# Performance work log

Hardware: AMD Instinct MI355X
Metric: run time of the kernel (lower is better)

The kernel has to match this reference:

```python
import jax, jax.numpy as jnp
import numpy as np

N, E, G = 50000, 800000, 64
IN_DIM, HID, HEADS = 128, 64, 4
EPS = 1e-5
NEG_SLOPE = 0.2


def _gatv2(x, src, dst, Wl, bl, Wr, br, att, bias, heads, ch):
    n = x.shape[0]
    xl = (x @ Wl + bl).reshape(n, heads, ch)
    xr = (x @ Wr + br).reshape(n, heads, ch)
    # edge-wise gather + GATv2 attention logits
    e = jax.nn.leaky_relu(xl[src] + xr[dst], NEG_SLOPE)          # [E,H,C]
    logits = jnp.einsum('ehc,hc->eh', e, att)                    # [E,H]
    # segment softmax over incoming edges of each destination node
    m = jax.ops.segment_max(logits, dst, num_segments=n)
    a = jnp.exp(logits - m[dst])
    denom = jax.ops.segment_sum(a, dst, num_segments=n)
    alpha = a / denom[dst]                                       # [E,H]
    out = jax.ops.segment_sum(alpha[:, :, None] * xl[src], dst, num_segments=n)
    return out.reshape(n, heads * ch) + bias


def _batchnorm(x, gamma, beta):
    mu = jnp.mean(x, axis=0)
    var = jnp.var(x, axis=0)
    return gamma * (x - mu) * jax.lax.rsqrt(var + EPS) + beta


def setup_inputs() -> dict:
    key = jax.random.key(0)
    ks = jax.random.split(key, 24)
    d1 = HID * HEADS  # 256
    def g(k, shape, scale):
        return jax.random.normal(k, shape, dtype=jnp.float32) * scale
    return {
        'x': g(ks[0], (N, IN_DIM), 1.0),
        'edge_index': jax.random.randint(ks[1], (2, E), 0, N, dtype=jnp.int32),
        'batch': jnp.sort(jax.random.randint(ks[2], (N,), 0, G, dtype=jnp.int32)),
        # conv1
        'W1l': g(ks[3], (IN_DIM, d1), 0.08), 'b1l': jnp.zeros((d1,), jnp.float32),
        'W1r': g(ks[4], (IN_DIM, d1), 0.08), 'b1r': jnp.zeros((d1,), jnp.float32),
        'att1': g(ks[5], (HEADS, HID), 0.1), 'bias1': jnp.zeros((d1,), jnp.float32),
        'gamma1': jnp.ones((d1,), jnp.float32), 'beta1': jnp.zeros((d1,), jnp.float32),
        # conv2 (heads=1)
        'W2l': g(ks[6], (d1, HID), 0.06), 'b2l': jnp.zeros((HID,), jnp.float32),
        'W2r': g(ks[7], (d1, HID), 0.06), 'b2r': jnp.zeros((HID,), jnp.float32),
        'att2': g(ks[8], (1, HID), 0.1), 'bias2': jnp.zeros((HID,), jnp.float32),
        'gamma2': jnp.ones((HID,), jnp.float32), 'beta2': jnp.zeros((HID,), jnp.float32),
        # MLP head
        'lw1': g(ks[9], (HID, HID), 0.12), 'lb1': jnp.zeros((HID,), jnp.float32),
        'lw2': g(ks[10], (HID, 1), 0.12), 'lb2': jnp.zeros((1,), jnp.float32),
    }


def reference(x, edge_index, batch, W1l, b1l, W1r, b1r, att1, bias1, gamma1, beta1,
              W2l, b2l, W2r, b2r, att2, bias2, gamma2, beta2, lw1, lb1, lw2, lb2):
    n = x.shape[0]
    loops = jnp.arange(n, dtype=edge_index.dtype)
    src = jnp.concatenate([edge_index[0], loops])
    dst = jnp.concatenate([edge_index[1], loops])

    h = _gatv2(x, src, dst, W1l, b1l, W1r, b1r, att1, bias1, HEADS, HID)
    h = jax.nn.elu(_batchnorm(h, gamma1, beta1))
    # dropout: identity in eval mode
    h = _gatv2(h, src, dst, W2l, b2l, W2r, b2r, att2, bias2, 1, HID)
    h = jax.nn.elu(_batchnorm(h, gamma2, beta2))

    # global mean pool over graphs
    sums = jax.ops.segment_sum(h, batch, num_segments=G)
    cnts = jax.ops.segment_sum(jnp.ones((n, 1), h.dtype), batch, num_segments=G)
    pooled = sums / jnp.maximum(cnts, 1.0)

    out = jax.nn.elu(pooled @ lw1 + lb1)
    return out @ lw2 + lb2
```

## Files before the change

kernel.cpp:

```cpp
#include <hip/hip_runtime.h>
#include <hip/hip_bf16.h>

#define NN 50000
#define NE 800000
#define ET (NE + NN)
#define NG 64
#define IND 128
#define HD 64
#define NH 4
#define D1 256
#define BN_EPS 1e-5f
#define SLOPE 0.2f
#define PW_NODES 25
#define LOG2E 1.4426950408889634f

typedef unsigned short u16;
typedef __attribute__((ext_vector_type(8))) short bf16x8;
typedef __attribute__((ext_vector_type(4))) float f32x4;

__device__ __forceinline__ float b2f(u16 u){
  union { unsigned int i; float f; } c; c.i = ((unsigned int)u) << 16; return c.f;
}
__device__ __forceinline__ u16 f2b(float f){
  unsigned int u = __float_as_uint(f);
  u = (u + 0x7FFF + ((u >> 16) & 1)) >> 16;
  return (u16)u;
}

__global__ void k_cvt(const float* __restrict__ x, u16* __restrict__ xb, int n4){
  int i = blockIdx.x*256 + threadIdx.x;
  if (i >= n4) return;
  float4 v = reinterpret_cast<const float4*>(x)[i];
  ushort4 o; o.x = f2b(v.x); o.y = f2b(v.y); o.z = f2b(v.z); o.w = f2b(v.w);
  reinterpret_cast<ushort4*>(xb)[i] = o;
}

__global__ void k_wprep(const float* __restrict__ Wa, const float* __restrict__ Wb,
                        u16* __restrict__ Wt, int KT, int NOUT){
  int id = blockIdx.x*256 + threadIdx.x;
  int total = 2*NOUT*(KT/4);
  if (id >= total) return;
  int c  = id % (2*NOUT);
  int k4 = (id / (2*NOUT))*4;
  const float* W = (c < NOUT) ? Wa : Wb;
  int cl = (c < NOUT) ? c : c - NOUT;
  ushort4 o;
  o.x = f2b(W[(size_t)(k4+0)*NOUT + cl]);
  o.y = f2b(W[(size_t)(k4+1)*NOUT + cl]);
  o.z = f2b(W[(size_t)(k4+2)*NOUT + cl]);
  o.w = f2b(W[(size_t)(k4+3)*NOUT + cl]);
  *reinterpret_cast<ushort4*>(&Wt[(size_t)c*KT + k4]) = o;
}

__global__ void k_count(const int* __restrict__ ei, int* __restrict__ cnt){
  int e = blockIdx.x*256 + threadIdx.x;
  if (e >= ET) return;
  int d = (e < NE) ? ei[NE + e] : (e - NE);
  atomicAdd(&cnt[d], 1);
}

__global__ __launch_bounds__(1024) void k_scan1(const int* __restrict__ cnt,
                                                int* __restrict__ ro, int* __restrict__ part){
  __shared__ int s[1024];
  int i = blockIdx.x*1024 + threadIdx.x;
  int v = (i < NN) ? cnt[i] : 0;
  s[threadIdx.x] = v;
  __syncthreads();
  for (int off = 1; off < 1024; off <<= 1){
    int t = (threadIdx.x >= off) ? s[threadIdx.x - off] : 0;
    __syncthreads();
    s[threadIdx.x] += t;
    __syncthreads();
  }
  if (i < NN) ro[i] = s[threadIdx.x] - v;
  if (threadIdx.x == 1023) part[blockIdx.x] = s[1023];
}

__global__ __launch_bounds__(64) void k_scan2(int* __restrict__ part, int nb){
  __shared__ int s[64];
  int v = (threadIdx.x < nb) ? part[threadIdx.x] : 0;
  s[threadIdx.x] = v;
  __syncthreads();
  for (int off = 1; off < 64; off <<= 1){
    int t = (threadIdx.x >= off) ? s[threadIdx.x - off] : 0;
    __syncthreads();
    s[threadIdx.x] += t;
    __syncthreads();
  }
  if (threadIdx.x < nb) part[threadIdx.x] = s[threadIdx.x] - v;
}

__global__ __launch_bounds__(1024) void k_scan3(const int* __restrict__ part, int* __restrict__ ro){
  int i = blockIdx.x*1024 + threadIdx.x;
  if (i < NN) ro[i] += part[blockIdx.x];
  if (i == 0) ro[NN] = ET;
}

__global__ void k_scatter(const int* __restrict__ ei, const int* __restrict__ ro,
                          int* __restrict__ cur, int* __restrict__ ssrc){
  int e = blockIdx.x*256 + threadIdx.x;
  if (e >= ET) return;
  int s, d;
  if (e < NE){ s = ei[e]; d = ei[NE + e]; } else { s = e - NE; d = s; }
  int pos = ro[d] + atomicAdd(&cur[d], 1);
  ssrc[pos] = s;
}

template<int KT, int NOUT>
__global__ __launch_bounds__(256) void k_gemm(const u16* __restrict__ Ab,
      const u16* __restrict__ Wt, const float* __restrict__ ba, const float* __restrict__ bb,
      u16* __restrict__ Ca, u16* __restrict__ Cb){
  __shared__ u16 As[64][32];
  __shared__ u16 Bs[128][32];
  int t = threadIdx.x;
  int lane = t & 63;
  int w = t >> 6;
  int wm = w >> 1, wn = w & 1;
  int n0 = blockIdx.x*64;
  int cb0 = blockIdx.y*128;

  f32x4 acc[2][4];
  #pragma unroll
  for (int i = 0; i < 2; i++)
    #pragma unroll
    for (int j = 0; j < 4; j++) acc[i][j] = (f32x4){0.f,0.f,0.f,0.f};

  int sr = t >> 3;
  int k4 = (t & 7)*4;
  int fm = lane & 15;
  int fk = (lane >> 4)*8;

  for (int kb = 0; kb < KT/32; kb++){
    int kbase = kb*32;
    #pragma unroll
    for (int p = 0; p < 2; p++){
      int r = sr + p*32;
      int gn = n0 + r;
      ushort4 v = make_ushort4(0,0,0,0);
      if (gn < NN) v = *reinterpret_cast<const ushort4*>(&Ab[(size_t)gn*KT + kbase + k4]);
      *reinterpret_cast<ushort4*>(&As[r][k4]) = v;
    }
    #pragma unroll
    for (int q = 0; q < 4; q++){
      int cn = sr + q*32;
      ushort4 v = *reinterpret_cast<const ushort4*>(&Wt[(size_t)(cb0+cn)*KT + kbase + k4]);
      *reinterpret_cast<ushort4*>(&Bs[cn][k4]) = v;
    }
    __syncthreads();
    bf16x8 af0 = *reinterpret_cast<const bf16x8*>(&As[wm*32 + fm][fk]);
    bf16x8 af1 = *reinterpret_cast<const bf16x8*>(&As[wm*32 + 16 + fm][fk]);
    #pragma unroll
    for (int nt = 0; nt < 4; nt++){
      bf16x8 bfr = *reinterpret_cast<const bf16x8*>(&Bs[wn*64 + nt*16 + fm][fk]);
      acc[0][nt] = __builtin_amdgcn_mfma_f32_16x16x32_bf16(af0, bfr, acc[0][nt], 0, 0, 0);
      acc[1][nt] = __builtin_amdgcn_mfma_f32_16x16x32_bf16(af1, bfr, acc[1][nt], 0, 0, 0);
    }
    __syncthreads();
  }

  int frow = (lane >> 4)*4;
  #pragma unroll
  for (int nt = 0; nt < 4; nt++){
    int cn = cb0 + wn*64 + nt*16 + fm;
    bool first = (cn < NOUT);
    int cl = first ? cn : cn - NOUT;
    float bv = first ? ba[cl] : bb[cl];
    u16* Cp = first ? Ca : Cb;
    #pragma unroll
    for (int mt = 0; mt < 2; mt++){
      #pragma unroll
      for (int r = 0; r < 4; r++){
        int grow = n0 + wm*32 + mt*16 + frow + r;
        if (grow < NN) Cp[(size_t)grow*NOUT + cl] = f2b(acc[mt][nt][r] + bv);
      }
    }
  }
}

__global__ __launch_bounds__(256) void k_gat1(const int* __restrict__ ro, const int* __restrict__ ssrc,
      const u16* __restrict__ xl, const u16* __restrict__ xr,
      const float* __restrict__ att, const float* __restrict__ bias,
      u16* __restrict__ out){
  int widx = threadIdx.x >> 6, lane = threadIdx.x & 63;
  int n = blockIdx.x*4 + widx;
  if (n >= NN) return;
  int base = (lane >> 4)*HD + (lane & 15)*4;
  ushort4 ur = *reinterpret_cast<const ushort4*>(&xr[(size_t)n*D1 + base]);
  float xr0 = b2f(ur.x), xr1 = b2f(ur.y), xr2 = b2f(ur.z), xr3 = b2f(ur.w);
  float4 at4 = *reinterpret_cast<const float4*>(&att[base]);
  float a1x = 0.6f*LOG2E*at4.x, a2x = 0.4f*LOG2E*at4.x;
  float a1y = 0.6f*LOG2E*at4.y, a2y = 0.4f*LOG2E*at4.y;
  float a1z = 0.6f*LOG2E*at4.z, a2z = 0.4f*LOG2E*at4.z;
  float a1w = 0.6f*LOG2E*at4.w, a2w = 0.4f*LOG2E*at4.w;
  float m = -1e30f, den = 0.f;
  float ax=0.f, ay=0.f, az=0.f, aw=0.f;
  int b = ro[n], e = ro[n+1];
  int i = b;
  for (; i + 3 < e; i += 4){
    int s0 = ssrc[i], s1 = ssrc[i+1], s2 = ssrc[i+2], s3 = ssrc[i+3];
    ushort4 u0 = *reinterpret_cast<const ushort4*>(&xl[(size_t)s0*D1 + base]);
    ushort4 u1 = *reinterpret_cast<const ushort4*>(&xl[(size_t)s1*D1 + base]);
    ushort4 u2 = *reinterpret_cast<const ushort4*>(&xl[(size_t)s2*D1 + base]);
    ushort4 u3 = *reinterpret_cast<const ushort4*>(&xl[(size_t)s3*D1 + base]);
    float v0x=b2f(u0.x), v0y=b2f(u0.y), v0z=b2f(u0.z), v0w=b2f(u0.w);
    float v1x=b2f(u1.x), v1y=b2f(u1.y), v1z=b2f(u1.z), v1w=b2f(u1.w);
    float v2x=b2f(u2.x), v2y=b2f(u2.y), v2z=b2f(u2.z), v2w=b2f(u2.w);
    float v3x=b2f(u3.x), v3y=b2f(u3.y), v3z=b2f(u3.z), v3w=b2f(u3.w);
    float t0, t1, t2, t3;
    float L0, L1, L2, L3;
    t0 = v0x+xr0; t1 = v0y+xr1; t2 = v0z+xr2; t3 = v0w+xr3;
    L0 = fmaf(a1x,t0, a2x*fabsf(t0));
    L0 = fmaf(a1y,t1, fmaf(a2y,fabsf(t1), L0));
    L0 = fmaf(a1z,t2, fmaf(a2z,fabsf(t2), L0));
    L0 = fmaf(a1w,t3, fmaf(a2w,fabsf(t3), L0));
    t0 = v1x+xr0; t1 = v1y+xr1; t2 = v1z+xr2; t3 = v1w+xr3;
    L1 = fmaf(a1x,t0, a2x*fabsf(t0));
    L1 = fmaf(a1y,t1, fmaf(a2y,fabsf(t1), L1));
    L1 = fmaf(a1z,t2, fmaf(a2z,fabsf(t2), L1));
    L1 = fmaf(a1w,t3, fmaf(a2w,fabsf(t3), L1));
    t0 = v2x+xr0; t1 = v2y+xr1; t2 = v2z+xr2; t3 = v2w+xr3;
    L2 = fmaf(a1x,t0, a2x*fabsf(t0));
    L2 = fmaf(a1y,t1, fmaf(a2y,fabsf(t1), L2));
    L2 = fmaf(a1z,t2, fmaf(a2z,fabsf(t2), L2));
    L2 = fmaf(a1w,t3, fmaf(a2w,fabsf(t3), L2));
    t0 = v3x+xr0; t1 = v3y+xr1; t2 = v3z+xr2; t3 = v3w+xr3;
    L3 = fmaf(a1x,t0, a2x*fabsf(t0));
    L3 = fmaf(a1y,t1, fmaf(a2y,fabsf(t1), L3));
    L3 = fmaf(a1z,t2, fmaf(a2z,fabsf(t2), L3));
    L3 = fmaf(a1w,t3, fmaf(a2w,fabsf(t3), L3));
    #pragma unroll
    for (int off = 1; off <= 8; off <<= 1){
      L0 += __shfl_xor(L0, off); L1 += __shfl_xor(L1, off);
      L2 += __shfl_xor(L2, off); L3 += __shfl_xor(L3, off);
    }
    float Lm = fmaxf(fmaxf(L0, L1), fmaxf(L2, L3));
    if (__any(Lm > m + 8.f)){
      float mn = fmaxf(m, Lm);
      float corr = exp2f(m - mn);
      den *= corr; ax *= corr; ay *= corr; az *= corr; aw *= corr;
      m = mn;
    }
    float p0 = exp2f(L0 - m), p1 = exp2f(L1 - m);
    float p2 = exp2f(L2 - m), p3 = exp2f(L3 - m);
    den += (p0 + p1) + (p2 + p3);
    ax = fmaf(p0,v0x, fmaf(p1,v1x, fmaf(p2,v2x, fmaf(p3,v3x, ax))));
    ay = fmaf(p0,v0y, fmaf(p1,v1y, fmaf(p2,v2y, fmaf(p3,v3y, ay))));
    az = fmaf(p0,v0z, fmaf(p1,v1z, fmaf(p2,v2z, fmaf(p3,v3z, az))));
    aw = fmaf(p0,v0w, fmaf(p1,v1w, fmaf(p2,v2w, fmaf(p3,v3w, aw))));
  }
  for (; i < e; i++){
    int s = ssrc[i];
    ushort4 u = *reinterpret_cast<const ushort4*>(&xl[(size_t)s*D1 + base]);
    float vx = b2f(u.x), vy = b2f(u.y), vz = b2f(u.z), vw = b2f(u.w);
    float t0 = vx + xr0, t1 = vy + xr1, t2 = vz + xr2, t3 = vw + xr3;
    float L;
    L = fmaf(a1x, t0, a2x*fabsf(t0));
    L = fmaf(a1y, t1, fmaf(a2y, fabsf(t1), L));
    L = fmaf(a1z, t2, fmaf(a2z, fabsf(t2), L));
    L = fmaf(a1w, t3, fmaf(a2w, fabsf(t3), L));
    L += __shfl_xor(L, 1); L += __shfl_xor(L, 2);
    L += __shfl_xor(L, 4); L += __shfl_xor(L, 8);
    if (__any(L > m + 8.f)){
      float mn = fmaxf(m, L);
      float corr = exp2f(m - mn);
      den *= corr; ax *= corr; ay *= corr; az *= corr; aw *= corr;
      m = mn;
    }
    float p = exp2f(L - m);
    den += p;
    ax = fmaf(p, vx, ax);
    ay = fmaf(p, vy, ay);
    az = fmaf(p, vz, az);
    aw = fmaf(p, vw, aw);
  }
  float inv = 1.f/den;
  float4 b4 = *reinterpret_cast<const float4*>(&bias[base]);
  ushort4 o;
  o.x = f2b(ax*inv + b4.x); o.y = f2b(ay*inv + b4.y);
  o.z = f2b(az*inv + b4.z); o.w = f2b(aw*inv + b4.w);
  *reinterpret_cast<ushort4*>(&out[(size_t)n*D1 + base]) = o;
}

__global__ __launch_bounds__(256) void k_bnstats16(const u16* __restrict__ h, float* __restrict__ stats,
                                                   int ncols, int rpb){
  int nrl = 256/ncols;
  int c = threadIdx.x % ncols;
  int rl = threadIdx.x / ncols;
  int r0 = blockIdx.x*rpb + rl;
  int r1 = min(NN, (blockIdx.x+1)*rpb);
  float s = 0.f, s2 = 0.f;
  for (int r = r0; r < r1; r += nrl){
    float v = b2f(h[(size_t)r*ncols + c]);
    s += v; s2 += v*v;
  }
  atomicAdd(&stats[c], s);
  atomicAdd(&stats[ncols + c], s2);
}

__global__ __launch_bounds__(256) void k_bnstats(const float* __restrict__ h, float* __restrict__ stats,
                                                 int ncols, int rpb){
  int nrl = 256/ncols;
  int c = threadIdx.x % ncols;
  int rl = threadIdx.x / ncols;
  int r0 = blockIdx.x*rpb + rl;
  int r1 = min(NN, (blockIdx.x+1)*rpb);
  float s = 0.f, s2 = 0.f;
  for (int r = r0; r < r1; r += nrl){
    float v = h[(size_t)r*ncols + c];
    s += v; s2 += v*v;
  }
  atomicAdd(&stats[c], s);
  atomicAdd(&stats[ncols + c], s2);
}

__global__ void k_bn1b(u16* __restrict__ h, const float* __restrict__ stats,
                       const float* __restrict__ gamma, const float* __restrict__ beta){
  const float invn = 1.f/NN;
  size_t total = (size_t)NN*D1/4;
  for (size_t i = (size_t)blockIdx.x*blockDim.x + threadIdx.x; i < total;
       i += (size_t)gridDim.x*blockDim.x){
    int c4 = (int)((i & (D1/4 - 1))*4);
    ushort4 u = reinterpret_cast<ushort4*>(h)[i];
    ushort4 o;
    #pragma unroll
    for (int j = 0; j < 4; j++){
      int c = c4 + j;
      float mu = stats[c]*invn;
      float var = stats[D1 + c]*invn - mu*mu;
      float g = gamma[c]*rsqrtf(var + BN_EPS);
      u16 uj = (j==0)?u.x:(j==1)?u.y:(j==2)?u.z:u.w;
      float v = (b2f(uj) - mu)*g + beta[c];
      v = (v > 0.f) ? v : (__expf(v) - 1.f);
      u16 ov = f2b(v);
      if (j==0) o.x = ov; else if (j==1) o.y = ov; else if (j==2) o.z = ov; else o.w = ov;
    }
    reinterpret_cast<ushort4*>(h)[i] = o;
  }
}

__global__ __launch_bounds__(256) void k_gat2(const int* __restrict__ ro, const int* __restrict__ ssrc,
      const u16* __restrict__ xl, const u16* __restrict__ xr,
      const float* __restrict__ att, const float* __restrict__ bias,
      float* __restrict__ out){
  int widx = threadIdx.x >> 6, lane = threadIdx.x & 63;
  int n = blockIdx.x*4 + widx;
  if (n >= NN) return;
  int g = lane >> 4, c4 = (lane & 15)*4;
  ushort4 ur = *reinterpret_cast<const ushort4*>(&xr[(size_t)n*HD + c4]);
  float xr0 = b2f(ur.x), xr1 = b2f(ur.y), xr2 = b2f(ur.z), xr3 = b2f(ur.w);
  float4 at4 = *reinterpret_cast<const float4*>(&att[c4]);
  float a1x = 0.6f*LOG2E*at4.x, a2x = 0.4f*LOG2E*at4.x;
  float a1y = 0.6f*LOG2E*at4.y, a2y = 0.4f*LOG2E*at4.y;
  float a1z = 0.6f*LOG2E*at4.z, a2z = 0.4f*LOG2E*at4.z;
  float a1w = 0.6f*LOG2E*at4.w, a2w = 0.4f*LOG2E*at4.w;
  float m = -1e30f, den = 0.f;
  float ax=0.f, ay=0.f, az=0.f, aw=0.f;
  int b = ro[n], e = ro[n+1];
  int i = b + g;
  for (; i + 4 < e; i += 8){
    int s0 = ssrc[i], s1 = ssrc[i+4];
    ushort4 u0 = *reinterpret_cast<const ushort4*>(&xl[(size_t)s0*HD + c4]);
    ushort4 u1 = *reinterpret_cast<const ushort4*>(&xl[(size_t)s1*HD + c4]);
    float v0x=b2f(u0.x), v0y=b2f(u0.y), v0z=b2f(u0.z), v0w=b2f(u0.w);
    float v1x=b2f(u1.x), v1y=b2f(u1.y), v1z=b2f(u1.z), v1w=b2f(u1.w);
    float t0, t1, t2, t3, L0, L1;
    t0 = v0x+xr0; t1 = v0y+xr1; t2 = v0z+xr2; t3 = v0w+xr3;
    L0 = fmaf(a1x,t0, a2x*fabsf(t0));
    L0 = fmaf(a1y,t1, fmaf(a2y,fabsf(t1), L0));
    L0 = fmaf(a1z,t2, fmaf(a2z,fabsf(t2), L0));
    L0 = fmaf(a1w,t3, fmaf(a2w,fabsf(t3), L0));
    t0 = v1x+xr0; t1 = v1y+xr1; t2 = v1z+xr2; t3 = v1w+xr3;
    L1 = fmaf(a1x,t0, a2x*fabsf(t0));
    L1 = fmaf(a1y,t1, fmaf(a2y,fabsf(t1), L1));
    L1 = fmaf(a1z,t2, fmaf(a2z,fabsf(t2), L1));
    L1 = fmaf(a1w,t3, fmaf(a2w,fabsf(t3), L1));
    #pragma unroll
    for (int off = 1; off <= 8; off <<= 1){
      L0 += __shfl_xor(L0, off); L1 += __shfl_xor(L1, off);
    }
    float Lm = fmaxf(L0, L1);
    if (__any(Lm > m + 8.f)){
      float mn = fmaxf(m, Lm);
      float corr = exp2f(m - mn);
      den *= corr; ax *= corr; ay *= corr; az *= corr; aw *= corr;
      m = mn;
    }
    float p0 = exp2f(L0 - m), p1 = exp2f(L1 - m);
    den += p0 + p1;
    ax = fmaf(p0, v0x, fmaf(p1, v1x, ax));
    ay = fmaf(p0, v0y, fmaf(p1, v1y, ay));
    az = fmaf(p0, v0z, fmaf(p1, v1z, az));
    aw = fmaf(p0, v0w, fmaf(p1, v1w, aw));
  }
  for (; i < e; i += 4){
    int s = ssrc[i];
    ushort4 u = *reinterpret_cast<const ushort4*>(&xl[(size_t)s*HD + c4]);
    float vx = b2f(u.x), vy = b2f(u.y), vz = b2f(u.z), vw = b2f(u.w);
    float t0 = vx + xr0, t1 = vy + xr1, t2 = vz + xr2, t3 = vw + xr3;
    float L;
    L = fmaf(a1x, t0, a2x*fabsf(t0));
    L = fmaf(a1y, t1, fmaf(a2y, fabsf(t1), L));
    L = fmaf(a1z, t2, fmaf(a2z, fabsf(t2), L));
    L = fmaf(a1w, t3, fmaf(a2w, fabsf(t3), L));
    L += __shfl_xor(L, 1); L += __shfl_xor(L, 2);
    L += __shfl_xor(L, 4); L += __shfl_xor(L, 8);
    if (__any(L > m + 8.f)){
      float mn = fmaxf(m, L);
      float corr = exp2f(m - mn);
      den *= corr; ax *= corr; ay *= corr; az *= corr; aw *= corr;
      m = mn;
    }
    float p = exp2f(L - m);
    den += p;
    ax = fmaf(p, vx, ax);
    ay = fmaf(p, vy, ay);
    az = fmaf(p, vz, az);
    aw = fmaf(p, vw, aw);
  }
  #pragma unroll
  for (int off = 16; off <= 32; off <<= 1){
    float mo  = __shfl_xor(m, off);
    float dno = __shfl_xor(den, off);
    float bx  = __shfl_xor(ax, off);
    float by  = __shfl_xor(ay, off);
    float bz  = __shfl_xor(az, off);
    float bw  = __shfl_xor(aw, off);
    float mn = fmaxf(m, mo);
    float c1 = exp2f(m - mn), c2 = exp2f(mo - mn);
    den = den*c1 + dno*c2;
    ax = ax*c1 + bx*c2;
    ay = ay*c1 + by*c2;
    az = az*c1 + bz*c2;
    aw = aw*c1 + bw*c2;
    m = mn;
  }
  float inv = 1.f/den;
  float4 b4 = *reinterpret_cast<const float4*>(&bias[c4]);
  float4 o = make_float4(ax*inv + b4.x, ay*inv + b4.y, az*inv + b4.z, aw*inv + b4.w);
  *reinterpret_cast<float4*>(&out[(size_t)n*HD + c4]) = o;
}

__global__ __launch_bounds__(256) void k_bn2pool(const float* __restrict__ h2, const float* __restrict__ stats,
      const float* __restrict__ gamma, const float* __restrict__ beta,
      const int* __restrict__ batch, float* __restrict__ pool, float* __restrict__ pcnt){
  int wave = blockIdx.x*4 + (threadIdx.x >> 6);
  int lane = threadIdx.x & 63;
  int n0 = wave*PW_NODES;
  if (n0 >= NN) return;
  int n1 = min(NN, n0 + PW_NODES);
  const float invn = 1.f/NN;
  float mu = stats[lane]*invn;
  float var = stats[HD + lane]*invn - mu*mu;
  float sc = gamma[lane]*rsqrtf(var + BN_EPS);
  float sh = beta[lane] - mu*sc;
  int curg = batch[n0];
  float acc = 0.f, cnt = 0.f;
  for (int n = n0; n < n1; n++){
    int g = batch[n];
    if (g != curg){
      atomicAdd(&pool[curg*HD + lane], acc);
      if (lane == 0) atomicAdd(&pcnt[curg], cnt);
      acc = 0.f; cnt = 0.f; curg = g;
    }
    float v = h2[(size_t)n*HD + lane]*sc + sh;
    v = (v > 0.f) ? v : (__expf(v) - 1.f);
    acc += v; cnt += 1.f;
  }
  atomicAdd(&pool[curg*HD + lane], acc);
  if (lane == 0) atomicAdd(&pcnt[curg], cnt);
}

__global__ __launch_bounds__(64) void k_mlp(const float* __restrict__ pool, const float* __restrict__ pcnt,
      const float* __restrict__ lw1, const float* __restrict__ lb1,
      const float* __restrict__ lw2, const float* __restrict__ lb2, float* __restrict__ out){
  __shared__ float p[HD];
  int g = blockIdx.x, c = threadIdx.x;
  float cnt = fmaxf(pcnt[g], 1.f);
  p[c] = pool[g*HD + c]/cnt;
  __syncthreads();
  float acc = lb1[c];
  for (int k = 0; k < HD; k++) acc += p[k]*lw1[k*HD + c];
  acc = (acc > 0.f) ? acc : (__expf(acc) - 1.f);
  float t = acc * lw2[c];
  #pragma unroll
  for (int off = 32; off > 0; off >>= 1) t += __shfl_xor(t, off, 64);
  if (c == 0) out[g] = t + lb2[0];
}

extern "C" void kernel_launch(void* const* d_in, const int* in_sizes, int n_in,
                              void* d_out, int out_size, void* d_ws, size_t ws_size,
                              hipStream_t stream){
  const float* x    = (const float*)d_in[0];
  const int*  ei    = (const int*) d_in[1];
  const int*  batch = (const int*) d_in[2];
  const float* W1l = (const float*)d_in[3];
  const float* b1l = (const float*)d_in[4];
  const float* W1r = (const float*)d_in[5];
  const float* b1r = (const float*)d_in[6];
  const float* att1= (const float*)d_in[7];
  const float* bias1=(const float*)d_in[8];
  const float* gamma1=(const float*)d_in[9];
  const float* beta1 =(const float*)d_in[10];
  const float* W2l = (const float*)d_in[11];
  const float* b2l = (const float*)d_in[12];
  const float* W2r = (const float*)d_in[13];
  const float* b2r = (const float*)d_in[14];
  const float* att2= (const float*)d_in[15];
  const float* bias2=(const float*)d_in[16];
  const float* gamma2=(const float*)d_in[17];
  const float* beta2 =(const float*)d_in[18];
  const float* lw1 = (const float*)d_in[19];
  const float* lb1 = (const float*)d_in[20];
  const float* lw2 = (const float*)d_in[21];
  const float* lb2 = (const float*)d_in[22];
  float* out = (float*)d_out;

  char* w = (char*)d_ws;
  size_t off = 0;
  auto take = [&](size_t bytes)->char*{
    char* p = w + off;
    off = (off + bytes + 255) & ~(size_t)255;
    return p;
  };
  int*   ro    = (int*)  take((NN+1)*sizeof(int));
  int*   cur   = (int*)  take((size_t)NN*sizeof(int));
  int*   ssrc  = (int*)  take((size_t)ET*sizeof(int));
  int*   part  = (int*)  take(64*sizeof(int));
  float* stats1= (float*)take(2*D1*sizeof(float));
  float* stats2= (float*)take(2*HD*sizeof(float));
  float* pool  = (float*)take(NG*HD*sizeof(float));
  float* pcnt  = (float*)take(NG*sizeof(float));
  u16*   xb    = (u16*)  take((size_t)NN*IND*sizeof(u16));
  u16*   Wt1   = (u16*)  take((size_t)2*D1*IND*sizeof(u16));
  u16*   Wt2   = (u16*)  take((size_t)2*HD*D1*sizeof(u16));
  char*  bufA  = take((size_t)NN*D1*2*sizeof(u16));
  u16*   h1    = (u16*)  take((size_t)NN*D1*sizeof(u16));

  u16* xlb1 = (u16*)bufA;
  u16* xrb1 = xlb1 + (size_t)NN*D1;
  u16* xlb2 = (u16*)bufA;
  u16* xrb2 = xlb2 + (size_t)NN*HD;
  float* h2 = (float*)(bufA + (size_t)2*NN*HD*sizeof(u16));

  k_cvt<<<(NN*IND/4 + 255)/256, 256, 0, stream>>>(x, xb, NN*IND/4);
  k_wprep<<<(2*D1*(IND/4) + 255)/256, 256, 0, stream>>>(W1l, W1r, Wt1, IND, D1);
  k_wprep<<<(2*HD*(D1/4) + 255)/256, 256, 0, stream>>>(W2l, W2r, Wt2, D1, HD);

  hipMemsetAsync(cur, 0, (size_t)NN*sizeof(int), stream);
  k_count<<<(ET+255)/256, 256, 0, stream>>>(ei, cur);
  int nsb = (NN + 1023)/1024;
  k_scan1<<<nsb, 1024, 0, stream>>>(cur, ro, part);
  k_scan2<<<1, 64, 0, stream>>>(part, nsb);
  k_scan3<<<nsb, 1024, 0, stream>>>(part, ro);
  hipMemsetAsync(cur, 0, (size_t)NN*sizeof(int), stream);
  k_scatter<<<(ET+255)/256, 256, 0, stream>>>(ei, ro, cur, ssrc);

  const int MB = (NN + 63)/64;

  k_gemm<IND, D1><<<dim3(MB, 4), 256, 0, stream>>>(xb, Wt1, b1l, b1r, xlb1, xrb1);
  k_gat1<<<(NN+3)/4, 256, 0, stream>>>(ro, ssrc, xlb1, xrb1, att1, bias1, h1);
  hipMemsetAsync(stats1, 0, 2*D1*sizeof(float), stream);
  k_bnstats16<<<196, 256, 0, stream>>>(h1, stats1, D1, 256);
  k_bn1b<<<2048, 256, 0, stream>>>(h1, stats1, gamma1, beta1);

  k_gemm<D1, HD><<<dim3(MB, 1), 256, 0, stream>>>(h1, Wt2, b2l, b2r, xlb2, xrb2);
  k_gat2<<<(NN+3)/4, 256, 0, stream>>>(ro, ssrc, xlb2, xrb2, att2, bias2, h2);
  hipMemsetAsync(stats2, 0, 2*HD*sizeof(float), stream);
  k_bnstats<<<196, 256, 0, stream>>>(h2, stats2, HD, 256);

  hipMemsetAsync(pool, 0, NG*HD*sizeof(float), stream);
  hipMemsetAsync(pcnt, 0, NG*sizeof(float), stream);
  {
    int waves = (NN + PW_NODES - 1)/PW_NODES;
    int blocks = (waves + 3)/4;
    k_bn2pool<<<blocks, 256, 0, stream>>>(h2, stats2, gamma2, beta2, batch, pool, pcnt);
  }
  k_mlp<<<NG, 64, 0, stream>>>(pool, pcnt, lw1, lb1, lw2, lb2, out);
}
```

Baseline: 412.5 us.

## Merge prep kernels and memsets, single-block scan, fuse BN1+ELU into GEMM2 load

Folds the input/weight conversions and all workspace zeroing into one prep kernel, which removes several launches and memset calls. The three-kernel CSR scan becomes a single 1024-thread block that also re-zeroes the counters. The standalone BN1+ELU pass over h1 is removed: the second GEMM computes per-column scale and shift into shared memory and applies normalization and ELU while loading its A tiles. This saves a full read-write pass over the hidden activations, at the cost of a serial single-block scan and extra ALU work inside the GEMM load path.

```diff
diff --git a/kernel.cpp b/kernel.cpp
--- a/kernel.cpp
+++ b/kernel.cpp
@@ -27,29 +27,63 @@
   return (u16)u;
 }
 
-__global__ void k_cvt(const float* __restrict__ x, u16* __restrict__ xb, int n4){
-  int i = blockIdx.x*256 + threadIdx.x;
-  if (i >= n4) return;
-  float4 v = reinterpret_cast<const float4*>(x)[i];
-  ushort4 o; o.x = f2b(v.x); o.y = f2b(v.y); o.z = f2b(v.z); o.w = f2b(v.w);
-  reinterpret_cast<ushort4*>(xb)[i] = o;
-}
-
-__global__ void k_wprep(const float* __restrict__ Wa, const float* __restrict__ Wb,
-                        u16* __restrict__ Wt, int KT, int NOUT){
+#define PX   (NN*IND/4)
+#define PW1  (2*D1*(IND/4))
+#define PW2  (2*HD*(D1/4))
+#define PZC  NN
+#define PZS  (2*D1 + 2*HD + NG*HD + NG)
+#define PTOT (PX + PW1 + PW2 + PZC + PZS)
+
+__global__ void k_prep(const float* __restrict__ x, u16* __restrict__ xb,
+      const float* __restrict__ W1a, const float* __restrict__ W1b, u16* __restrict__ Wt1,
+      const float* __restrict__ W2a, const float* __restrict__ W2b, u16* __restrict__ Wt2,
+      int* __restrict__ cur, float* __restrict__ stats1, float* __restrict__ stats2,
+      float* __restrict__ pool, float* __restrict__ pcnt){
   int id = blockIdx.x*256 + threadIdx.x;
-  int total = 2*NOUT*(KT/4);
-  if (id >= total) return;
-  int c  = id % (2*NOUT);
-  int k4 = (id / (2*NOUT))*4;
-  const float* W = (c < NOUT) ? Wa : Wb;
-  int cl = (c < NOUT) ? c : c - NOUT;
-  ushort4 o;
-  o.x = f2b(W[(size_t)(k4+0)*NOUT + cl]);
-  o.y = f2b(W[(size_t)(k4+1)*NOUT + cl]);
-  o.z = f2b(W[(size_t)(k4+2)*NOUT + cl]);
-  o.w = f2b(W[(size_t)(k4+3)*NOUT + cl]);
-  *reinterpret_cast<ushort4*>(&Wt[(size_t)c*KT + k4]) = o;
+  if (id < PX){
+    float4 v = reinterpret_cast<const float4*>(x)[id];
+    ushort4 o; o.x = f2b(v.x); o.y = f2b(v.y); o.z = f2b(v.z); o.w = f2b(v.w);
+    reinterpret_cast<ushort4*>(xb)[id] = o;
+    return;
+  }
+  id -= PX;
+  if (id < PW1){
+    int c  = id % (2*D1);
+    int k4 = (id / (2*D1))*4;
+    const float* W = (c < D1) ? W1a : W1b;
+    int cl = (c < D1) ? c : c - D1;
+    ushort4 o;
+    o.x = f2b(W[(size_t)(k4+0)*D1 + cl]);
+    o.y = f2b(W[(size_t)(k4+1)*D1 + cl]);
+    o.z = f2b(W[(size_t)(k4+2)*D1 + cl]);
+    o.w = f2b(W[(size_t)(k4+3)*D1 + cl]);
+    *reinterpret_cast<ushort4*>(&Wt1[(size_t)c*IND + k4]) = o;
+    return;
+  }
+  id -= PW1;
+  if (id < PW2){
+    int c  = id % (2*HD);
+    int k4 = (id / (2*HD))*4;
+    const float* W = (c < HD) ? W2a : W2b;
+    int cl = (c < HD) ? c : c - HD;
+    ushort4 o;
+    o.x = f2b(W[(size_t)(k4+0)*HD + cl]);
+    o.y = f2b(W[(size_t)(k4+1)*HD + cl]);
+    o.z = f2b(W[(size_t)(k4+2)*HD + cl]);
+    o.w = f2b(W[(size_t)(k4+3)*HD + cl]);
+    *reinterpret_cast<ushort4*>(&Wt2[(size_t)c*D1 + k4]) = o;
+    return;
+  }
+  id -= PW2;
+  if (id < PZC){ cur[id] = 0; return; }
+  id -= PZC;
+  if (id < 2*D1){ stats1[id] = 0.f; return; }
+  id -= 2*D1;
+  if (id < 2*HD){ stats2[id] = 0.f; return; }
+  id -= 2*HD;
+  if (id < NG*HD){ pool[id] = 0.f; return; }
+  id -= NG*HD;
+  if (id < NG) pcnt[id] = 0.f;
 }
 
 __global__ void k_count(const int* __restrict__ ei, int* __restrict__ cnt){
@@ -59,41 +93,35 @@
   atomicAdd(&cnt[d], 1);
 }
 
-__global__ __launch_bounds__(1024) void k_scan1(const int* __restrict__ cnt,
-                                                int* __restrict__ ro, int* __restrict__ part){
+__global__ __launch_bounds__(1024) void k_scan(int* __restrict__ cur, int* __restrict__ ro){
   __shared__ int s[1024];
-  int i = blockIdx.x*1024 + threadIdx.x;
-  int v = (i < NN) ? cnt[i] : 0;
-  s[threadIdx.x] = v;
+  const int CH = (NN + 1023)/1024;
+  int t = threadIdx.x;
+  int base = t*CH;
+  int sum = 0;
+  for (int i = 0; i < CH; i++){
+    int idx = base + i;
+    if (idx < NN) sum += cur[idx];
+  }
+  s[t] = sum;
   __syncthreads();
   for (int off = 1; off < 1024; off <<= 1){
-    int t = (threadIdx.x >= off) ? s[threadIdx.x - off] : 0;
+    int v = (t >= off) ? s[t - off] : 0;
     __syncthreads();
-    s[threadIdx.x] += t;
+    s[t] += v;
     __syncthreads();
   }
-  if (i < NN) ro[i] = s[threadIdx.x] - v;
-  if (threadIdx.x == 1023) part[blockIdx.x] = s[1023];
-}
-
-__global__ __launch_bounds__(64) void k_scan2(int* __restrict__ part, int nb){
-  __shared__ int s[64];
-  int v = (threadIdx.x < nb) ? part[threadIdx.x] : 0;
-  s[threadIdx.x] = v;
-  __syncthreads();
-  for (int off = 1; off < 64; off <<= 1){
-    int t = (threadIdx.x >= off) ? s[threadIdx.x - off] : 0;
-    __syncthreads();
-    s[threadIdx.x] += t;
-    __syncthreads();
-  }
-  if (threadIdx.x < nb) part[threadIdx.x] = s[threadIdx.x] - v;
-}
-
-__global__ __launch_bounds__(1024) void k_scan3(const int* __restrict__ part, int* __restrict__ ro){
-  int i = blockIdx.x*1024 + threadIdx.x;
-  if (i < NN) ro[i] += part[blockIdx.x];
-  if (i == 0) ro[NN] = ET;
+  int pre = s[t] - sum;
+  for (int i = 0; i < CH; i++){
+    int idx = base + i;
+    if (idx < NN){
+      int c = cur[idx];
+      ro[idx] = pre;
+      pre += c;
+      cur[idx] = 0;
+    }
+  }
+  if (t == 1023) ro[NN] = ET;
 }
 
 __global__ void k_scatter(const int* __restrict__ ei, const int* __restrict__ ro,
@@ -106,12 +134,15 @@
   ssrc[pos] = s;
 }
 
-template<int KT, int NOUT>
+template<int KT, int NOUT, bool BN>
 __global__ __launch_bounds__(256) void k_gemm(const u16* __restrict__ Ab,
       const u16* __restrict__ Wt, const float* __restrict__ ba, const float* __restrict__ bb,
+      const float* __restrict__ stats, const float* __restrict__ gamma, const float* __restrict__ beta,
       u16* __restrict__ Ca, u16* __restrict__ Cb){
   __shared__ u16 As[64][32];
   __shared__ u16 Bs[128][32];
+  __shared__ float scl[KT];
+  __shared__ float shl[KT];
   int t = threadIdx.x;
   int lane = t & 63;
   int w = t >> 6;
@@ -119,6 +150,17 @@
   int n0 = blockIdx.x*64;
   int cb0 = blockIdx.y*128;
 
+  if constexpr (BN){
+    for (int c = t; c < KT; c += 256){
+      float mu = stats[c]*(1.f/NN);
+      float var = stats[KT + c]*(1.f/NN) - mu*mu;
+      float g = gamma[c]*rsqrtf(var + BN_EPS);
+      scl[c] = g;
+      shl[c] = beta[c] - mu*g;
+    }
+    __syncthreads();
+  }
+
   f32x4 acc[2][4];
   #pragma unroll
   for (int i = 0; i < 2; i++)
@@ -138,6 +180,14 @@
       int gn = n0 + r;
       ushort4 v = make_ushort4(0,0,0,0);
       if (gn < NN) v = *reinterpret_cast<const ushort4*>(&Ab[(size_t)gn*KT + kbase + k4]);
+      if constexpr (BN){
+        int c0 = kbase + k4;
+        float f0 = b2f(v.x)*scl[c0+0] + shl[c0+0]; f0 = (f0 > 0.f) ? f0 : (__expf(f0) - 1.f);
+        float f1 = b2f(v.y)*scl[c0+1] + shl[c0+1]; f1 = (f1 > 0.f) ? f1 : (__expf(f1) - 1.f);
+        float f2 = b2f(v.z)*scl[c0+2] + shl[c0+2]; f2 = (f2 > 0.f) ? f2 : (__expf(f2) - 1.f);
+        float f3 = b2f(v.w)*scl[c0+3] + shl[c0+3]; f3 = (f3 > 0.f) ? f3 : (__expf(f3) - 1.f);
+        v.x = f2b(f0); v.y = f2b(f1); v.z = f2b(f2); v.w = f2b(f3);
+      }
       *reinterpret_cast<ushort4*>(&As[r][k4]) = v;
     }
     #pragma unroll
@@ -313,31 +363,6 @@
   atomicAdd(&stats[ncols + c], s2);
 }
 
-__global__ void k_bn1b(u16* __restrict__ h, const float* __restrict__ stats,
-                       const float* __restrict__ gamma, const float* __restrict__ beta){
-  const float invn = 1.f/NN;
-  size_t total = (size_t)NN*D1/4;
-  for (size_t i = (size_t)blockIdx.x*blockDim.x + threadIdx.x; i < total;
-       i += (size_t)gridDim.x*blockDim.x){
-    int c4 = (int)((i & (D1/4 - 1))*4);
-    ushort4 u = reinterpret_cast<ushort4*>(h)[i];
-    ushort4 o;
-    #pragma unroll
-    for (int j = 0; j < 4; j++){
-      int c = c4 + j;
-      float mu = stats[c]*invn;
-      float var = stats[D1 + c]*invn - mu*mu;
-      float g = gamma[c]*rsqrtf(var + BN_EPS);
-      u16 uj = (j==0)?u.x:(j==1)?u.y:(j==2)?u.z:u.w;
-      float v = (b2f(uj) - mu)*g + beta[c];
-      v = (v > 0.f) ? v : (__expf(v) - 1.f);
-      u16 ov = f2b(v);
-      if (j==0) o.x = ov; else if (j==1) o.y = ov; else if (j==2) o.z = ov; else o.w = ov;
-    }
-    reinterpret_cast<ushort4*>(h)[i] = o;
-  }
-}
-
 __global__ __launch_bounds__(256) void k_gat2(const int* __restrict__ ro, const int* __restrict__ ssrc,
       const u16* __restrict__ xl, const u16* __restrict__ xr,
       const float* __restrict__ att, const float* __restrict__ bias,
@@ -525,7 +550,6 @@
   int*   ro    = (int*)  take((NN+1)*sizeof(int));
   int*   cur   = (int*)  take((size_t)NN*sizeof(int));
   int*   ssrc  = (int*)  take((size_t)ET*sizeof(int));
-  int*   part  = (int*)  take(64*sizeof(int));
   float* stats1= (float*)take(2*D1*sizeof(float));
   float* stats2= (float*)take(2*HD*sizeof(float));
   float* pool  = (float*)take(NG*HD*sizeof(float));
@@ -542,34 +566,25 @@
   u16* xrb2 = xlb2 + (size_t)NN*HD;
   float* h2 = (float*)(bufA + (size_t)2*NN*HD*sizeof(u16));
 
-  k_cvt<<<(NN*IND/4 + 255)/256, 256, 0, stream>>>(x, xb, NN*IND/4);
-  k_wprep<<<(2*D1*(IND/4) + 255)/256, 256, 0, stream>>>(W1l, W1r, Wt1, IND, D1);
-  k_wprep<<<(2*HD*(D1/4) + 255)/256, 256, 0, stream>>>(W2l, W2r, Wt2, D1, HD);
-
-  hipMemsetAsync(cur, 0, (size_t)NN*sizeof(int), stream);
+  k_prep<<<(PTOT + 255)/256, 256, 0, stream>>>(x, xb, W1l, W1r, Wt1, W2l, W2r, Wt2,
+                                               cur, stats1, stats2, pool, pcnt);
+
   k_count<<<(ET+255)/256, 256, 0, stream>>>(ei, cur);
-  int nsb = (NN + 1023)/1024;
-  k_scan1<<<nsb, 1024, 0, stream>>>(cur, ro, part);
-  k_scan2<<<1, 64, 0, stream>>>(part, nsb);
-  k_scan3<<<nsb, 1024, 0, stream>>>(part, ro);
-  hipMemsetAsync(cur, 0, (size_t)NN*sizeof(int), stream);
+  k_scan<<<1, 1024, 0, stream>>>(cur, ro);
   k_scatter<<<(ET+255)/256, 256, 0, stream>>>(ei, ro, cur, ssrc);
 
   const int MB = (NN + 63)/64;
 
-  k_gemm<IND, D1><<<dim3(MB, 4), 256, 0, stream>>>(xb, Wt1, b1l, b1r, xlb1, xrb1);
+  k_gemm<IND, D1, false><<<dim3(MB, 4), 256, 0, stream>>>(xb, Wt1, b1l, b1r,
+        nullptr, nullptr, nullptr, xlb1, xrb1);
   k_gat1<<<(NN+3)/4, 256, 0, stream>>>(ro, ssrc, xlb1, xrb1, att1, bias1, h1);
-  hipMemsetAsync(stats1, 0, 2*D1*sizeof(float), stream);
   k_bnstats16<<<196, 256, 0, stream>>>(h1, stats1, D1, 256);
-  k_bn1b<<<2048, 256, 0, stream>>>(h1, stats1, gamma1, beta1);
-
-  k_gemm<D1, HD><<<dim3(MB, 1), 256, 0, stream>>>(h1, Wt2, b2l, b2r, xlb2, xrb2);
+
+  k_gemm<D1, HD, true><<<dim3(MB, 1), 256, 0, stream>>>(h1, Wt2, b2l, b2r,
+        stats1, gamma1, beta1, xlb2, xrb2);
   k_gat2<<<(NN+3)/4, 256, 0, stream>>>(ro, ssrc, xlb2, xrb2, att2, bias2, h2);
-  hipMemsetAsync(stats2, 0, 2*HD*sizeof(float), stream);
   k_bnstats<<<196, 256, 0, stream>>>(h2, stats2, HD, 256);
 
-  hipMemsetAsync(pool, 0, NG*HD*sizeof(float), stream);
-  hipMemsetAsync(pcnt, 0, NG*sizeof(float), stream);
   {
     int waves = (NN + PW_NODES - 1)/PW_NODES;
     int blocks = (waves + 3)/4;
```

After: 503.6 us. 1.22x slower.
